# Optimization experiments

Hardware: AMD Instinct MI355X
Metric: run time of the kernel (lower is better)

The kernel has to match this reference:

```python
import jax, jax.numpy as jnp
import numpy as np

N_NODES = 200000
N_EDGES = 4000000
NUM_BASIS = 10
MAX_RADIUS = 1.0
NUM_NEIGHBORS = 10
HIDDEN = 16
# e3nn FCTP(0e+1o+2e, 0e+1o+2e -> 0e): 3 paths (l x l -> 0e), path coeff = 1/sqrt(n_paths*(2l+1))
PATH_C = np.array([1.0 / np.sqrt(3.0 * (2 * l + 1)) for l in (0, 1, 2)], dtype=np.float32)


def _spherical_harmonics_l2(v):
    """e3nn spherical harmonics lmax=2, normalize=True, 'component' normalization. v: [E,3] -> [E,9]."""
    r = jnp.linalg.norm(v, axis=-1, keepdims=True)
    u = v / jnp.maximum(r, 1e-12)
    x, y, z = u[:, 0], u[:, 1], u[:, 2]
    s3, s5 = np.sqrt(3.0).astype(np.float32), np.sqrt(5.0).astype(np.float32)
    sh0 = jnp.ones_like(x)[:, None]                      # [E,1]
    sh1 = s3 * u                                         # [E,3]
    x2, y2, z2 = x * x, y * y, z * z
    sh2 = s5 * jnp.stack([s3 * x * z,
                          s3 * x * y,
                          y2 - 0.5 * (x2 + z2),
                          s3 * y * z,
                          0.5 * s3 * (z2 - x2)], axis=-1)  # [E,5]
    return jnp.concatenate([sh0, sh1, sh2], axis=-1)


def _radial_embedding(r):
    """e3nn soft_one_hot_linspace(basis='smooth_finite', cutoff=True) * sqrt(num_basis). r: [E] -> [E,NUM_BASIS]."""
    values = jnp.linspace(0.0, MAX_RADIUS, NUM_BASIS + 2)[1:-1]
    step = MAX_RADIUS / (NUM_BASIS + 1)
    diff = (r[:, None] - values) / step

    def soft_unit_step(t):
        return jnp.where(t > 0, jnp.exp(-1.0 / jnp.where(t > 0, t, 1.0)), 0.0)

    y = np.float32(1.14136 * np.exp(2.0)) * soft_unit_step(diff + 1.0) * soft_unit_step(1.0 - diff)
    return y * np.float32(np.sqrt(NUM_BASIS))


def setup_inputs() -> dict:
    key = jax.random.key(0)
    k1, k2, k3, k4, k5, k6 = jax.random.split(key, 6)
    node_feats = jax.random.normal(k1, (N_NODES, 9), dtype=jnp.float32)
    edge_vec = 0.25 * jax.random.normal(k2, (N_EDGES, 3), dtype=jnp.float32)  # keep norms mostly < max_radius
    edge_src = jax.random.randint(k3, (N_EDGES,), 0, N_NODES)
    edge_dst = jax.random.randint(k4, (N_EDGES,), 0, N_NODES)
    W1 = jax.random.normal(k5, (NUM_BASIS, HIDDEN), dtype=jnp.float32)
    W2 = jax.random.normal(k6, (HIDDEN, 3), dtype=jnp.float32)
    return {"node_feats": node_feats, "edge_vec": edge_vec, "W1": W1, "W2": W2,
            "edge_src": edge_src, "edge_dst": edge_dst}


def reference(node_feats, edge_vec, W1, W2, edge_src, edge_dst):
    r = jnp.linalg.norm(edge_vec, axis=-1)                      # [E]
    sh = _spherical_harmonics_l2(edge_vec)                      # [E,9]
    emb = _radial_embedding(r)                                  # [E,NUM_BASIS]
    # e3nn FullyConnectedNet([num_basis, 16, 3], relu): variance-preserving layers
    h = np.float32(np.sqrt(2.0)) * jax.nn.relu(emb @ W1 / np.float32(np.sqrt(NUM_BASIS)))
    w = h @ W2 / np.float32(np.sqrt(HIDDEN))                    # [E,3] per-edge TP weights
    f = node_feats[edge_src]                                    # gather [E,9]
    # FCTP paths: l x l -> 0e reduces to per-l dot products
    dots = jnp.stack([f[:, 0] * sh[:, 0],
                      jnp.sum(f[:, 1:4] * sh[:, 1:4], axis=-1),
                      jnp.sum(f[:, 4:9] * sh[:, 4:9], axis=-1)], axis=-1)  # [E,3]
    edge_out = jnp.sum(w * jnp.asarray(PATH_C) * dots, axis=-1)            # [E]
    node_out = jax.ops.segment_sum(edge_out, edge_dst, num_segments=N_NODES)
    node_out = node_out / np.float32(np.sqrt(NUM_NEIGHBORS))
    return node_out.sum()
```

## Files before the change

### kernel.cpp

```cpp
#include <hip/hip_runtime.h>
#include <hip/hip_fp16.h>

#define NTHREADS 256
#define NBLOCKS 2048
#define FB_NBLOCKS 2048
#define NB 1024
#define NBP 1040

#define KTOT 11.9269705f
#define CL0  0.04564355f
#define CL1  0.02635231f
#define CL2  0.02041241f
#define S3   1.7320508f
#define S5   2.2360680f

__device__ __forceinline__ float fast_rcp(float x) { return __builtin_amdgcn_rcpf(x); }

__global__ __launch_bounds__(256) void pack_feats_14(
    const float* __restrict__ nf, uint4* __restrict__ tab, int n_nodes)
{
    const int n = blockIdx.x * 256 + threadIdx.x;
    if (n >= n_nodes) return;
    const float* f = nf + 9 * (size_t)n;
    const float scale[9] = { 1.0f, S3, S3, S3, S5 * S3, S5 * S3, S5, S5 * S3,
                             0.5f * S5 * S3 };
    unsigned short hs[9];
#pragma unroll
    for (int i = 0; i < 9; ++i) {
        const __half h = __float2half_rn(f[i] * scale[i]);
        hs[i] = *reinterpret_cast<const unsigned short*>(&h);
    }
    unsigned long long c[9];
#pragma unroll
    for (int i = 1; i < 9; ++i)
        c[i] = (unsigned long long)(((unsigned)hs[i] + 2u) >> 2) & 0x3FFFull;
    const unsigned long long lo =
        c[1] | (c[2] << 14) | (c[3] << 28) | (c[4] << 42) | (c[5] << 56);
    const unsigned long long hi =
        (c[5] >> 8) | (c[6] << 6) | (c[7] << 20) | (c[8] << 34) |
        ((unsigned long long)hs[0] << 48);
    tab[n] = make_uint4((unsigned)lo, (unsigned)(lo >> 32),
                        (unsigned)hi, (unsigned)(hi >> 32));
}

__global__ __launch_bounds__(256) void build_wtable_kernel(
    const float* __restrict__ W1, const float* __restrict__ W2,
    float* __restrict__ wtabf)
{
    const int idx = blockIdx.x * 256 + threadIdx.x;
    if (idx > NB) return;
    const float r = (float)idx * (1.0f / (float)NB);

    const float t    = 11.0f * r;
    const int   k0   = (int)t;
    const float frac = t - (float)k0;
    float ea = 0.0f, eb = 0.0f;
    if (k0 >= 1 && k0 <= 10) {
        const float da = fmaf(-frac, frac, 1.0f);
        if (da > 0.0226f) ea = KTOT * __expf(-2.0f * fast_rcp(da));
    }
    if (k0 <= 9) {
        const float db = frac * (2.0f - frac);
        if (db > 0.0226f) eb = KTOT * __expf(-2.0f * fast_rcp(db));
    }
    const int ra = min(max(k0 - 1, 0), 9);
    const int rb = min(k0, 9);

    float w0 = 0.0f, w1 = 0.0f, w2 = 0.0f;
#pragma unroll
    for (int j = 0; j < 16; ++j) {
        const float h = fmaxf(fmaf(ea, W1[ra * 16 + j], eb * W1[rb * 16 + j]), 0.0f);
        w0 = fmaf(h, W2[j * 3 + 0], w0);
        w1 = fmaf(h, W2[j * 3 + 1], w1);
        w2 = fmaf(h, W2[j * 3 + 2], w2);
    }
    wtabf[idx]           = w0 * CL0;
    wtabf[NBP + idx]     = w1 * CL1;
    wtabf[2 * NBP + idx] = w2 * CL2;
}

__global__ __launch_bounds__(256) void build_wrec_kernel(
    const float* __restrict__ wtabf, uint4* __restrict__ wrec)
{
    const int i = blockIdx.x * 256 + threadIdx.x;
    if (i >= NB) return;
    const float w0a = wtabf[i],           w0b = wtabf[i + 1];
    const float w1a = wtabf[NBP + i],     w1b = wtabf[NBP + i + 1];
    const float w2a = wtabf[2 * NBP + i], w2b = wtabf[2 * NBP + i + 1];
    auto hbits = [](float v) -> unsigned {
        const __half h = __float2half_rn(v);
        return (unsigned)*reinterpret_cast<const unsigned short*>(&h);
    };
    const unsigned b0 = hbits(w0a), b1 = hbits(w1a), b2 = hbits(w2a);
    const unsigned d0 = hbits(w0b - w0a), d1 = hbits(w1b - w1a), d2 = hbits(w2b - w2a);
    wrec[i] = make_uint4(b0 | (b1 << 16), b2 | (d0 << 16), d1 | (d2 << 16), 0u);
}

__device__ __forceinline__ float cvt14(unsigned c) {
    __half_raw hr; hr.x = (unsigned short)(c << 2);
    return __half2float(*reinterpret_cast<const __half*>(&hr));
}
__device__ __forceinline__ float cvt16(unsigned c) {
    __half_raw hr; hr.x = (unsigned short)(c & 0xFFFFu);
    return __half2float(*reinterpret_cast<const __half*>(&hr));
}
__device__ __forceinline__ unsigned alignb(unsigned hi, unsigned lo, int s) {
    return (lo >> s) | (hi << (32 - s));
}

__device__ __forceinline__ float edge_term(
    float vx, float vy, float vz, uint4 g, const uint4* __restrict__ swq)
{
    const float r2 = fmaf(vx, vx, fmaf(vy, vy, vz * vz));
    const float rs = rsqrtf(fmaxf(r2, 1e-24f));
    const float r  = r2 * rs;
    const float x = vx * rs, y = vy * rs, z = vz * rs;

    const float tb = fminf(r, 1.0f) * (float)NB;
    const int   i  = min((int)tb, NB - 1);
    const float fb = tb - (float)i;
    const uint4 q = swq[i];
    const float wv0 = fmaf(fb, cvt16(q.y >> 16), cvt16(q.x));
    const float wv1 = fmaf(fb, cvt16(q.z),       cvt16(q.x >> 16));
    const float wv2 = fmaf(fb, cvt16(q.z >> 16), cvt16(q.y));

    const float fv1 = cvt14(g.x & 0x3FFFu);
    const float fv2 = cvt14((g.x >> 14) & 0x3FFFu);
    const float fv3 = cvt14(alignb(g.y, g.x, 28) & 0x3FFFu);
    const float fv4 = cvt14((g.y >> 10) & 0x3FFFu);
    const float fv5 = cvt14(alignb(g.z, g.y, 24) & 0x3FFFu);
    const float fv6 = cvt14((g.z >> 6) & 0x3FFFu);
    const float fv7 = cvt14(alignb(g.w, g.z, 20) & 0x3FFFu);
    const float fv8 = cvt14((g.w >> 2) & 0x3FFFu);
    const float f0  = cvt16(g.w >> 16);

    const float dots0 = f0;
    const float dots1 = fmaf(fv1, x, fmaf(fv2, y, fv3 * z));
    const float xx = x * x, yy = y * y, zz = z * z;
    const float dots2 = fmaf(fv4, x * z, fmaf(fv5, x * y,
                        fmaf(fv6, fmaf(-0.5f, xx + zz, yy),
                        fmaf(fv7, y * z, fv8 * (zz - xx)))));

    return fmaf(wv0, dots0, fmaf(wv1, dots1, wv2 * dots2));
}

__global__ __launch_bounds__(NTHREADS) void edge_sum_p14q(
    const float4* __restrict__ ev4,
    const int4*   __restrict__ src4,
    const uint4*  __restrict__ tab,
    const uint4*  __restrict__ wrec,
    float*        __restrict__ block_sums,
    int n_edges)
{
    __shared__ uint4 swq[NB];
    const int tid = threadIdx.x;
    for (int i = tid; i < NB; i += NTHREADS) swq[i] = wrec[i];
    __syncthreads();

    float acc = 0.0f;
    const int n_groups = (n_edges + 3) >> 2;
    const int stride = gridDim.x * blockDim.x;
    for (int g = blockIdx.x * blockDim.x + tid; g < n_groups; g += stride) {
        const int e0 = g << 2;
        if (e0 + 3 < n_edges) {
            const float4 a = ev4[3 * (size_t)g + 0];
            const float4 b = ev4[3 * (size_t)g + 1];
            const float4 c = ev4[3 * (size_t)g + 2];
            const int4   s = src4[g];
            const uint4 g0 = tab[s.x];
            const uint4 g1 = tab[s.y];
            const uint4 g2 = tab[s.z];
            const uint4 g3 = tab[s.w];
            acc += edge_term(a.x, a.y, a.z, g0, swq);
            acc += edge_term(a.w, b.x, b.y, g1, swq);
            acc += edge_term(b.z, b.w, c.x, g2, swq);
            acc += edge_term(c.y, c.z, c.w, g3, swq);
        } else {
            const float* evf  = reinterpret_cast<const float*>(ev4);
            const int*   srci = reinterpret_cast<const int*>(src4);
            for (int e = e0; e < n_edges; ++e) {
                acc += edge_term(evf[3 * (size_t)e], evf[3 * (size_t)e + 1],
                                 evf[3 * (size_t)e + 2], tab[srci[e]], swq);
            }
        }
    }

#pragma unroll
    for (int off = 1; off < 64; off <<= 1)
        acc += __shfl_xor(acc, off, 64);
    __shared__ float wsum[NTHREADS / 64];
    const int lane = tid & 63, wid = tid >> 6;
    if (lane == 0) wsum[wid] = acc;
    __syncthreads();
    if (tid == 0) {
        float ssum = 0.0f;
#pragma unroll
        for (int w = 0; w < NTHREADS / 64; ++w) ssum += wsum[w];
        block_sums[blockIdx.x] = ssum;
    }
}

__global__ __launch_bounds__(NTHREADS) void edge_sum_fallback(
    const float* __restrict__ node_feats,
    const float* __restrict__ edge_vec,
    const float* __restrict__ W1,
    const float* __restrict__ W2,
    const int*   __restrict__ edge_src,
    float*       __restrict__ block_sums,
    int n_edges)
{
    __shared__ float4 sW1[10][5];
    float* sW1f = reinterpret_cast<float*>(sW1);
    const int tid = threadIdx.x;
    if (tid < 160) {
        sW1f[(tid >> 4) * 20 + (tid & 15)] = W1[tid];
    } else if (tid < 200) {
        const int i = tid - 160;
        sW1f[(i >> 2) * 20 + 16 + (i & 3)] = 0.0f;
    }
    __syncthreads();

    float w2r[16][3];
#pragma unroll
    for (int j = 0; j < 16; ++j) {
        w2r[j][0] = W2[j * 3 + 0] * CL0;
        w2r[j][1] = W2[j * 3 + 1] * CL1;
        w2r[j][2] = W2[j * 3 + 2] * CL2;
    }

    float acc = 0.0f;
    const int stride = gridDim.x * blockDim.x;
    for (int e = blockIdx.x * blockDim.x + tid; e < n_edges; e += stride) {
        const float vx = edge_vec[3 * (size_t)e + 0];
        const float vy = edge_vec[3 * (size_t)e + 1];
        const float vz = edge_vec[3 * (size_t)e + 2];
        const int   src = edge_src[e];
        const float* f = node_feats + 9 * (size_t)src;
        const float r2 = fmaf(vx, vx, fmaf(vy, vy, vz * vz));
        const float rs = rsqrtf(fmaxf(r2, 1e-24f));
        const float r  = r2 * rs;
        const float x = vx * rs, y = vy * rs, z = vz * rs;
        const float t    = 11.0f * r;
        const int   k0   = (int)t;
        const float frac = t - (float)k0;
        float ea = 0.0f, eb = 0.0f;
        if (k0 >= 1 && k0 <= 10) {
            const float da = fmaf(-frac, frac, 1.0f);
            if (da > 0.0226f) ea = KTOT * __expf(-2.0f * fast_rcp(da));
        }
        if (k0 <= 9) {
            const float db = frac * (2.0f - frac);
            if (db > 0.0226f) eb = KTOT * __expf(-2.0f * fast_rcp(db));
        }
        const int ra = min(max(k0 - 1, 0), 9);
        const int rb = min(k0, 9);
        const float4* rowA = &sW1[ra][0];
        const float4* rowB = &sW1[rb][0];
        float wv0 = 0.0f, wv1 = 0.0f, wv2 = 0.0f;
#pragma unroll
        for (int q = 0; q < 4; ++q) {
            const float4 A = rowA[q];
            const float4 B = rowB[q];
            float h;
            h = fmaxf(fmaf(ea, A.x, eb * B.x), 0.0f);
            wv0 = fmaf(h, w2r[4 * q + 0][0], wv0); wv1 = fmaf(h, w2r[4 * q + 0][1], wv1); wv2 = fmaf(h, w2r[4 * q + 0][2], wv2);
            h = fmaxf(fmaf(ea, A.y, eb * B.y), 0.0f);
            wv0 = fmaf(h, w2r[4 * q + 1][0], wv0); wv1 = fmaf(h, w2r[4 * q + 1][1], wv1); wv2 = fmaf(h, w2r[4 * q + 1][2], wv2);
            h = fmaxf(fmaf(ea, A.z, eb * B.z), 0.0f);
            wv0 = fmaf(h, w2r[4 * q + 2][0], wv0); wv1 = fmaf(h, w2r[4 * q + 2][1], wv1); wv2 = fmaf(h, w2r[4 * q + 2][2], wv2);
            h = fmaxf(fmaf(ea, A.w, eb * B.w), 0.0f);
            wv0 = fmaf(h, w2r[4 * q + 3][0], wv0); wv1 = fmaf(h, w2r[4 * q + 3][1], wv1); wv2 = fmaf(h, w2r[4 * q + 3][2], wv2);
        }
        const float f0 = f[0], f1 = f[1], f2 = f[2], f3 = f[3], f4 = f[4];
        const float f5 = f[5], f6 = f[6], f7 = f[7], f8 = f[8];
        const float dots0 = f0;
        const float dots1 = S3 * fmaf(f1, x, fmaf(f2, y, f3 * z));
        const float xx = x * x, yy = y * y, zz = z * z;
        const float sh20 = S5 * S3 * x * z;
        const float sh21 = S5 * S3 * x * y;
        const float sh22 = S5 * (yy - 0.5f * (xx + zz));
        const float sh23 = S5 * S3 * y * z;
        const float sh24 = S5 * 0.5f * S3 * (zz - xx);
        const float dots2 = fmaf(f4, sh20, fmaf(f5, sh21, fmaf(f6, sh22, fmaf(f7, sh23, f8 * sh24))));
        acc = fmaf(wv0, dots0, acc);
        acc = fmaf(wv1, dots1, acc);
        acc = fmaf(wv2, dots2, acc);
    }
#pragma unroll
    for (int off = 1; off < 64; off <<= 1)
        acc += __shfl_xor(acc, off, 64);
    __shared__ float wsum[NTHREADS / 64];
    const int lane = tid & 63, wid = tid >> 6;
    if (lane == 0) wsum[wid] = acc;
    __syncthreads();
    if (tid == 0) {
        float ssum = 0.0f;
#pragma unroll
        for (int w = 0; w < NTHREADS / 64; ++w) ssum += wsum[w];
        block_sums[blockIdx.x] = ssum;
    }
}

__global__ __launch_bounds__(256) void final_reduce_kernel(
    const float* __restrict__ block_sums, float* __restrict__ out, int n)
{
    const int tid = threadIdx.x;
    float acc = 0.0f;
    for (int i = tid; i < n; i += 256) acc += block_sums[i];
#pragma unroll
    for (int off = 1; off < 64; off <<= 1)
        acc += __shfl_xor(acc, off, 64);
    __shared__ float wsum[4];
    if ((tid & 63) == 0) wsum[tid >> 6] = acc;
    __syncthreads();
    if (tid == 0) out[0] = wsum[0] + wsum[1] + wsum[2] + wsum[3];
}

extern "C" void kernel_launch(void* const* d_in, const int* in_sizes, int n_in,
                              void* d_out, int out_size, void* d_ws, size_t ws_size,
                              hipStream_t stream) {
    const float* node_feats = (const float*)d_in[0];
    const float* edge_vec   = (const float*)d_in[1];
    const float* W1         = (const float*)d_in[2];
    const float* W2         = (const float*)d_in[3];
    const int*   edge_src   = (const int*)d_in[4];
    const int n_edges = in_sizes[4];
    const int n_nodes = in_sizes[0] / 9;

    float* block_sums = (float*)d_ws;
    const size_t wtabf_off = 32768;
    const size_t wrec_off  = wtabf_off + ((3 * NBP * 4 + 255) & ~255);
    const size_t tab_off   = wrec_off + NB * 16;
    const size_t need      = tab_off + (size_t)n_nodes * 16;

    if (ws_size >= need) {
        float* wtabf = (float*)((char*)d_ws + wtabf_off);
        uint4* wrec  = (uint4*)((char*)d_ws + wrec_off);
        uint4* tab   = (uint4*)((char*)d_ws + tab_off);
        pack_feats_14<<<(n_nodes + 255) / 256, 256, 0, stream>>>(
            node_feats, tab, n_nodes);
        build_wtable_kernel<<<(NB + 256) / 256, 256, 0, stream>>>(W1, W2, wtabf);
        build_wrec_kernel<<<NB / 256, 256, 0, stream>>>(wtabf, wrec);
        edge_sum_p14q<<<NBLOCKS, NTHREADS, 0, stream>>>(
            (const float4*)edge_vec, (const int4*)edge_src, tab, wrec,
            block_sums, n_edges);
        final_reduce_kernel<<<1, 256, 0, stream>>>(block_sums, (float*)d_out, NBLOCKS);
    } else {
        edge_sum_fallback<<<FB_NBLOCKS, NTHREADS, 0, stream>>>(
            node_feats, edge_vec, W1, W2, edge_src, block_sums, n_edges);
        final_reduce_kernel<<<1, 256, 0, stream>>>(block_sums, (float*)d_out, FB_NBLOCKS);
    }
}
```

Before: 46.23 us.

## Fuse prep kernels into one launch and software-pipeline two edge groups

The three setup kernels (feature packing, weight table, and the fp16 base/delta LUT) become a single prep kernel. The LUT blocks recompute the MLP at both endpoints instead of reading an intermediate float table, which removes two launches and one buffer. The edge kernel now issues loads and gathers for its first two grid-stride groups before doing any math, to raise memory-level parallelism on the random node-table gathers. This costs more registers and duplicates the tail-handling code.

```diff
diff --git a/kernel.cpp b/kernel.cpp
--- a/kernel.cpp
+++ b/kernel.cpp
@@ -5,7 +5,6 @@
 #define NBLOCKS 2048
 #define FB_NBLOCKS 2048
 #define NB 1024
-#define NBP 1040
 
 #define KTOT 11.9269705f
 #define CL0  0.04564355f
@@ -16,41 +15,10 @@
 
 __device__ __forceinline__ float fast_rcp(float x) { return __builtin_amdgcn_rcpf(x); }
 
-__global__ __launch_bounds__(256) void pack_feats_14(
-    const float* __restrict__ nf, uint4* __restrict__ tab, int n_nodes)
-{
-    const int n = blockIdx.x * 256 + threadIdx.x;
-    if (n >= n_nodes) return;
-    const float* f = nf + 9 * (size_t)n;
-    const float scale[9] = { 1.0f, S3, S3, S3, S5 * S3, S5 * S3, S5, S5 * S3,
-                             0.5f * S5 * S3 };
-    unsigned short hs[9];
-#pragma unroll
-    for (int i = 0; i < 9; ++i) {
-        const __half h = __float2half_rn(f[i] * scale[i]);
-        hs[i] = *reinterpret_cast<const unsigned short*>(&h);
-    }
-    unsigned long long c[9];
-#pragma unroll
-    for (int i = 1; i < 9; ++i)
-        c[i] = (unsigned long long)(((unsigned)hs[i] + 2u) >> 2) & 0x3FFFull;
-    const unsigned long long lo =
-        c[1] | (c[2] << 14) | (c[3] << 28) | (c[4] << 42) | (c[5] << 56);
-    const unsigned long long hi =
-        (c[5] >> 8) | (c[6] << 6) | (c[7] << 20) | (c[8] << 34) |
-        ((unsigned long long)hs[0] << 48);
-    tab[n] = make_uint4((unsigned)lo, (unsigned)(lo >> 32),
-                        (unsigned)hi, (unsigned)(hi >> 32));
-}
-
-__global__ __launch_bounds__(256) void build_wtable_kernel(
-    const float* __restrict__ W1, const float* __restrict__ W2,
-    float* __restrict__ wtabf)
-{
-    const int idx = blockIdx.x * 256 + threadIdx.x;
-    if (idx > NB) return;
-    const float r = (float)idx * (1.0f / (float)NB);
-
+__device__ __forceinline__ void eval_w(
+    float r, const float* __restrict__ W1, const float* __restrict__ W2,
+    float& w0, float& w1, float& w2)
+{
     const float t    = 11.0f * r;
     const int   k0   = (int)t;
     const float frac = t - (float)k0;
@@ -65,8 +33,7 @@
     }
     const int ra = min(max(k0 - 1, 0), 9);
     const int rb = min(k0, 9);
-
-    float w0 = 0.0f, w1 = 0.0f, w2 = 0.0f;
+    w0 = 0.0f; w1 = 0.0f; w2 = 0.0f;
 #pragma unroll
     for (int j = 0; j < 16; ++j) {
         const float h = fmaxf(fmaf(ea, W1[ra * 16 + j], eb * W1[rb * 16 + j]), 0.0f);
@@ -74,26 +41,53 @@
         w1 = fmaf(h, W2[j * 3 + 1], w1);
         w2 = fmaf(h, W2[j * 3 + 2], w2);
     }
-    wtabf[idx]           = w0 * CL0;
-    wtabf[NBP + idx]     = w1 * CL1;
-    wtabf[2 * NBP + idx] = w2 * CL2;
-}
-
-__global__ __launch_bounds__(256) void build_wrec_kernel(
-    const float* __restrict__ wtabf, uint4* __restrict__ wrec)
-{
-    const int i = blockIdx.x * 256 + threadIdx.x;
-    if (i >= NB) return;
-    const float w0a = wtabf[i],           w0b = wtabf[i + 1];
-    const float w1a = wtabf[NBP + i],     w1b = wtabf[NBP + i + 1];
-    const float w2a = wtabf[2 * NBP + i], w2b = wtabf[2 * NBP + i + 1];
-    auto hbits = [](float v) -> unsigned {
-        const __half h = __float2half_rn(v);
-        return (unsigned)*reinterpret_cast<const unsigned short*>(&h);
-    };
-    const unsigned b0 = hbits(w0a), b1 = hbits(w1a), b2 = hbits(w2a);
-    const unsigned d0 = hbits(w0b - w0a), d1 = hbits(w1b - w1a), d2 = hbits(w2b - w2a);
-    wrec[i] = make_uint4(b0 | (b1 << 16), b2 | (d0 << 16), d1 | (d2 << 16), 0u);
+    w0 *= CL0; w1 *= CL1; w2 *= CL2;
+}
+
+__global__ __launch_bounds__(256) void prep_kernel(
+    const float* __restrict__ nf,
+    const float* __restrict__ W1, const float* __restrict__ W2,
+    uint4* __restrict__ tab, uint4* __restrict__ wrec,
+    int n_nodes, int pack_blocks)
+{
+    const int tid = threadIdx.x;
+    if ((int)blockIdx.x < pack_blocks) {
+        const int n = blockIdx.x * 256 + tid;
+        if (n >= n_nodes) return;
+        const float* f = nf + 9 * (size_t)n;
+        const float scale[9] = { 1.0f, S3, S3, S3, S5 * S3, S5 * S3, S5, S5 * S3,
+                                 0.5f * S5 * S3 };
+        unsigned short hs[9];
+#pragma unroll
+        for (int i = 0; i < 9; ++i) {
+            const __half h = __float2half_rn(f[i] * scale[i]);
+            hs[i] = *reinterpret_cast<const unsigned short*>(&h);
+        }
+        unsigned long long c[9];
+#pragma unroll
+        for (int i = 1; i < 9; ++i)
+            c[i] = (unsigned long long)(((unsigned)hs[i] + 2u) >> 2) & 0x3FFFull;
+        const unsigned long long lo =
+            c[1] | (c[2] << 14) | (c[3] << 28) | (c[4] << 42) | (c[5] << 56);
+        const unsigned long long hi =
+            (c[5] >> 8) | (c[6] << 6) | (c[7] << 20) | (c[8] << 34) |
+            ((unsigned long long)hs[0] << 48);
+        tab[n] = make_uint4((unsigned)lo, (unsigned)(lo >> 32),
+                            (unsigned)hi, (unsigned)(hi >> 32));
+    } else {
+        const int i = ((int)blockIdx.x - pack_blocks) * 256 + tid;
+        if (i >= NB) return;
+        float w0a, w1a, w2a, w0b, w1b, w2b;
+        eval_w((float)i       * (1.0f / (float)NB), W1, W2, w0a, w1a, w2a);
+        eval_w((float)(i + 1) * (1.0f / (float)NB), W1, W2, w0b, w1b, w2b);
+        auto hbits = [](float v) -> unsigned {
+            const __half h = __float2half_rn(v);
+            return (unsigned)*reinterpret_cast<const unsigned short*>(&h);
+        };
+        const unsigned b0 = hbits(w0a), b1 = hbits(w1a), b2 = hbits(w2a);
+        const unsigned d0 = hbits(w0b - w0a), d1 = hbits(w1b - w1a), d2 = hbits(w2b - w2a);
+        wrec[i] = make_uint4(b0 | (b1 << 16), b2 | (d0 << 16), d1 | (d2 << 16), 0u);
+    }
 }
 
 __device__ __forceinline__ float cvt14(unsigned c) {
@@ -144,7 +138,7 @@
     return fmaf(wv0, dots0, fmaf(wv1, dots1, wv2 * dots2));
 }
 
-__global__ __launch_bounds__(NTHREADS) void edge_sum_p14q(
+__global__ __launch_bounds__(NTHREADS) void edge_sum_u2(
     const float4* __restrict__ ev4,
     const int4*   __restrict__ src4,
     const uint4*  __restrict__ tab,
@@ -160,29 +154,77 @@
     float acc = 0.0f;
     const int n_groups = (n_edges + 3) >> 2;
     const int stride = gridDim.x * blockDim.x;
-    for (int g = blockIdx.x * blockDim.x + tid; g < n_groups; g += stride) {
+    const int g1 = blockIdx.x * blockDim.x + tid;
+    const int g2 = g1 + stride;
+    const bool v1 = (g1 < n_groups) && ((g1 << 2) + 4 <= n_edges);
+    const bool v2 = (g2 < n_groups) && ((g2 << 2) + 4 <= n_edges);
+
+    float4 a1, b1, c1, a2, b2, c2;
+    int4 s1, s2;
+    if (v1) {
+        a1 = ev4[3 * (size_t)g1 + 0];
+        b1 = ev4[3 * (size_t)g1 + 1];
+        c1 = ev4[3 * (size_t)g1 + 2];
+        s1 = src4[g1];
+    }
+    if (v2) {
+        a2 = ev4[3 * (size_t)g2 + 0];
+        b2 = ev4[3 * (size_t)g2 + 1];
+        c2 = ev4[3 * (size_t)g2 + 2];
+        s2 = src4[g2];
+    }
+    uint4 t0, t1, t2, t3, t4, t5, t6, t7;
+    if (v1) { t0 = tab[s1.x]; t1 = tab[s1.y]; t2 = tab[s1.z]; t3 = tab[s1.w]; }
+    if (v2) { t4 = tab[s2.x]; t5 = tab[s2.y]; t6 = tab[s2.z]; t7 = tab[s2.w]; }
+    if (v1) {
+        acc += edge_term(a1.x, a1.y, a1.z, t0, swq);
+        acc += edge_term(a1.w, b1.x, b1.y, t1, swq);
+        acc += edge_term(b1.z, b1.w, c1.x, t2, swq);
+        acc += edge_term(c1.y, c1.z, c1.w, t3, swq);
+    }
+    if (v2) {
+        acc += edge_term(a2.x, a2.y, a2.z, t4, swq);
+        acc += edge_term(a2.w, b2.x, b2.y, t5, swq);
+        acc += edge_term(b2.z, b2.w, c2.x, t6, swq);
+        acc += edge_term(c2.y, c2.z, c2.w, t7, swq);
+    }
+
+    for (int g = g1 + 2 * stride; g < n_groups; g += stride) {
         const int e0 = g << 2;
-        if (e0 + 3 < n_edges) {
+        if (e0 + 4 <= n_edges) {
             const float4 a = ev4[3 * (size_t)g + 0];
             const float4 b = ev4[3 * (size_t)g + 1];
             const float4 c = ev4[3 * (size_t)g + 2];
             const int4   s = src4[g];
-            const uint4 g0 = tab[s.x];
-            const uint4 g1 = tab[s.y];
-            const uint4 g2 = tab[s.z];
-            const uint4 g3 = tab[s.w];
-            acc += edge_term(a.x, a.y, a.z, g0, swq);
-            acc += edge_term(a.w, b.x, b.y, g1, swq);
-            acc += edge_term(b.z, b.w, c.x, g2, swq);
-            acc += edge_term(c.y, c.z, c.w, g3, swq);
+            const uint4 q0 = tab[s.x];
+            const uint4 q1 = tab[s.y];
+            const uint4 q2 = tab[s.z];
+            const uint4 q3 = tab[s.w];
+            acc += edge_term(a.x, a.y, a.z, q0, swq);
+            acc += edge_term(a.w, b.x, b.y, q1, swq);
+            acc += edge_term(b.z, b.w, c.x, q2, swq);
+            acc += edge_term(c.y, c.z, c.w, q3, swq);
         } else {
             const float* evf  = reinterpret_cast<const float*>(ev4);
             const int*   srci = reinterpret_cast<const int*>(src4);
-            for (int e = e0; e < n_edges; ++e) {
+            for (int e = e0; e < n_edges; ++e)
                 acc += edge_term(evf[3 * (size_t)e], evf[3 * (size_t)e + 1],
                                  evf[3 * (size_t)e + 2], tab[srci[e]], swq);
-            }
-        }
+        }
+    }
+    if (g1 < n_groups && !v1) {
+        const float* evf  = reinterpret_cast<const float*>(ev4);
+        const int*   srci = reinterpret_cast<const int*>(src4);
+        for (int e = (g1 << 2); e < n_edges; ++e)
+            acc += edge_term(evf[3 * (size_t)e], evf[3 * (size_t)e + 1],
+                             evf[3 * (size_t)e + 2], tab[srci[e]], swq);
+    }
+    if (g2 < n_groups && !v2) {
+        const float* evf  = reinterpret_cast<const float*>(ev4);
+        const int*   srci = reinterpret_cast<const int*>(src4);
+        for (int e = (g2 << 2); e < n_edges; ++e)
+            acc += edge_term(evf[3 * (size_t)e], evf[3 * (size_t)e + 1],
+                             evf[3 * (size_t)e + 2], tab[srci[e]], swq);
     }
 
 #pragma unroll
@@ -328,20 +370,18 @@
     const int n_nodes = in_sizes[0] / 9;
 
     float* block_sums = (float*)d_ws;
-    const size_t wtabf_off = 32768;
-    const size_t wrec_off  = wtabf_off + ((3 * NBP * 4 + 255) & ~255);
-    const size_t tab_off   = wrec_off + NB * 16;
-    const size_t need      = tab_off + (size_t)n_nodes * 16;
+    const size_t wrec_off = 32768;
+    const size_t tab_off  = wrec_off + NB * 16;
+    const size_t need     = tab_off + (size_t)n_nodes * 16;
 
     if (ws_size >= need) {
-        float* wtabf = (float*)((char*)d_ws + wtabf_off);
-        uint4* wrec  = (uint4*)((char*)d_ws + wrec_off);
-        uint4* tab   = (uint4*)((char*)d_ws + tab_off);
-        pack_feats_14<<<(n_nodes + 255) / 256, 256, 0, stream>>>(
-            node_feats, tab, n_nodes);
-        build_wtable_kernel<<<(NB + 256) / 256, 256, 0, stream>>>(W1, W2, wtabf);
-        build_wrec_kernel<<<NB / 256, 256, 0, stream>>>(wtabf, wrec);
-        edge_sum_p14q<<<NBLOCKS, NTHREADS, 0, stream>>>(
+        uint4* wrec = (uint4*)((char*)d_ws + wrec_off);
+        uint4* tab  = (uint4*)((char*)d_ws + tab_off);
+        const int pack_blocks = (n_nodes + 255) / 256;
+        const int lut_blocks  = NB / 256;
+        prep_kernel<<<pack_blocks + lut_blocks, 256, 0, stream>>>(
+            node_feats, W1, W2, tab, wrec, n_nodes, pack_blocks);
+        edge_sum_u2<<<NBLOCKS, NTHREADS, 0, stream>>>(
             (const float4*)edge_vec, (const int4*)edge_src, tab, wrec,
             block_sums, n_edges);
         final_reduce_kernel<<<1, 256, 0, stream>>>(block_sums, (float*)d_out, NBLOCKS);
```

Measured after the change: 44.80 us. 3.1% less time.

## Merge prep kernels into one launch, use nontemporal streaming loads and raw rsq

Applied to the files above, without the earlier changes.

Folds the node-feature packing, radial weight table build and delta-record build into a single prep kernel. The LUT blocks now evaluate the MLP directly at both interval ends instead of going through an intermediate float table. This removes two kernel launches and their serialisation gaps. The edge kernel reads edge vectors and source indices with nontemporal loads so the streaming data does not evict the gathered node table from cache, and it uses the raw v_rsq instruction instead of rsqrtf. The cost is duplicated MLP evaluation per LUT entry and a slight change in rsqrt accuracy.

```diff
diff --git a/kernel.cpp b/kernel.cpp
--- a/kernel.cpp
+++ b/kernel.cpp
@@ -5,7 +5,6 @@
 #define NBLOCKS 2048
 #define FB_NBLOCKS 2048
 #define NB 1024
-#define NBP 1040
 
 #define KTOT 11.9269705f
 #define CL0  0.04564355f
@@ -15,42 +14,27 @@
 #define S5   2.2360680f
 
 __device__ __forceinline__ float fast_rcp(float x) { return __builtin_amdgcn_rcpf(x); }
-
-__global__ __launch_bounds__(256) void pack_feats_14(
-    const float* __restrict__ nf, uint4* __restrict__ tab, int n_nodes)
-{
-    const int n = blockIdx.x * 256 + threadIdx.x;
-    if (n >= n_nodes) return;
-    const float* f = nf + 9 * (size_t)n;
-    const float scale[9] = { 1.0f, S3, S3, S3, S5 * S3, S5 * S3, S5, S5 * S3,
-                             0.5f * S5 * S3 };
-    unsigned short hs[9];
-#pragma unroll
-    for (int i = 0; i < 9; ++i) {
-        const __half h = __float2half_rn(f[i] * scale[i]);
-        hs[i] = *reinterpret_cast<const unsigned short*>(&h);
-    }
-    unsigned long long c[9];
-#pragma unroll
-    for (int i = 1; i < 9; ++i)
-        c[i] = (unsigned long long)(((unsigned)hs[i] + 2u) >> 2) & 0x3FFFull;
-    const unsigned long long lo =
-        c[1] | (c[2] << 14) | (c[3] << 28) | (c[4] << 42) | (c[5] << 56);
-    const unsigned long long hi =
-        (c[5] >> 8) | (c[6] << 6) | (c[7] << 20) | (c[8] << 34) |
-        ((unsigned long long)hs[0] << 48);
-    tab[n] = make_uint4((unsigned)lo, (unsigned)(lo >> 32),
-                        (unsigned)hi, (unsigned)(hi >> 32));
-}
-
-__global__ __launch_bounds__(256) void build_wtable_kernel(
-    const float* __restrict__ W1, const float* __restrict__ W2,
-    float* __restrict__ wtabf)
-{
-    const int idx = blockIdx.x * 256 + threadIdx.x;
-    if (idx > NB) return;
-    const float r = (float)idx * (1.0f / (float)NB);
-
+__device__ __forceinline__ float fast_rsq(float x) {
+    float r;
+    asm("v_rsq_f32 %0, %1" : "=v"(r) : "v"(x));
+    return r;
+}
+
+typedef float    vf4 __attribute__((ext_vector_type(4)));
+typedef int      vi4 __attribute__((ext_vector_type(4)));
+__device__ __forceinline__ float4 ntload4(const float4* p) {
+    vf4 v = __builtin_nontemporal_load((const vf4*)p);
+    return make_float4(v.x, v.y, v.z, v.w);
+}
+__device__ __forceinline__ int4 ntloadi4(const int4* p) {
+    vi4 v = __builtin_nontemporal_load((const vi4*)p);
+    return make_int4(v.x, v.y, v.z, v.w);
+}
+
+__device__ __forceinline__ void eval_w(
+    float r, const float* __restrict__ W1, const float* __restrict__ W2,
+    float& w0, float& w1, float& w2)
+{
     const float t    = 11.0f * r;
     const int   k0   = (int)t;
     const float frac = t - (float)k0;
@@ -65,8 +49,7 @@
     }
     const int ra = min(max(k0 - 1, 0), 9);
     const int rb = min(k0, 9);
-
-    float w0 = 0.0f, w1 = 0.0f, w2 = 0.0f;
+    w0 = 0.0f; w1 = 0.0f; w2 = 0.0f;
 #pragma unroll
     for (int j = 0; j < 16; ++j) {
         const float h = fmaxf(fmaf(ea, W1[ra * 16 + j], eb * W1[rb * 16 + j]), 0.0f);
@@ -74,26 +57,53 @@
         w1 = fmaf(h, W2[j * 3 + 1], w1);
         w2 = fmaf(h, W2[j * 3 + 2], w2);
     }
-    wtabf[idx]           = w0 * CL0;
-    wtabf[NBP + idx]     = w1 * CL1;
-    wtabf[2 * NBP + idx] = w2 * CL2;
-}
-
-__global__ __launch_bounds__(256) void build_wrec_kernel(
-    const float* __restrict__ wtabf, uint4* __restrict__ wrec)
-{
-    const int i = blockIdx.x * 256 + threadIdx.x;
-    if (i >= NB) return;
-    const float w0a = wtabf[i],           w0b = wtabf[i + 1];
-    const float w1a = wtabf[NBP + i],     w1b = wtabf[NBP + i + 1];
-    const float w2a = wtabf[2 * NBP + i], w2b = wtabf[2 * NBP + i + 1];
-    auto hbits = [](float v) -> unsigned {
-        const __half h = __float2half_rn(v);
-        return (unsigned)*reinterpret_cast<const unsigned short*>(&h);
-    };
-    const unsigned b0 = hbits(w0a), b1 = hbits(w1a), b2 = hbits(w2a);
-    const unsigned d0 = hbits(w0b - w0a), d1 = hbits(w1b - w1a), d2 = hbits(w2b - w2a);
-    wrec[i] = make_uint4(b0 | (b1 << 16), b2 | (d0 << 16), d1 | (d2 << 16), 0u);
+    w0 *= CL0; w1 *= CL1; w2 *= CL2;
+}
+
+__global__ __launch_bounds__(256) void prep_kernel(
+    const float* __restrict__ nf,
+    const float* __restrict__ W1, const float* __restrict__ W2,
+    uint4* __restrict__ tab, uint4* __restrict__ wrec,
+    int n_nodes, int pack_blocks)
+{
+    const int tid = threadIdx.x;
+    if ((int)blockIdx.x < pack_blocks) {
+        const int n = blockIdx.x * 256 + tid;
+        if (n >= n_nodes) return;
+        const float* f = nf + 9 * (size_t)n;
+        const float scale[9] = { 1.0f, S3, S3, S3, S5 * S3, S5 * S3, S5, S5 * S3,
+                                 0.5f * S5 * S3 };
+        unsigned short hs[9];
+#pragma unroll
+        for (int i = 0; i < 9; ++i) {
+            const __half h = __float2half_rn(f[i] * scale[i]);
+            hs[i] = *reinterpret_cast<const unsigned short*>(&h);
+        }
+        unsigned long long c[9];
+#pragma unroll
+        for (int i = 1; i < 9; ++i)
+            c[i] = (unsigned long long)(((unsigned)hs[i] + 2u) >> 2) & 0x3FFFull;
+        const unsigned long long lo =
+            c[1] | (c[2] << 14) | (c[3] << 28) | (c[4] << 42) | (c[5] << 56);
+        const unsigned long long hi =
+            (c[5] >> 8) | (c[6] << 6) | (c[7] << 20) | (c[8] << 34) |
+            ((unsigned long long)hs[0] << 48);
+        tab[n] = make_uint4((unsigned)lo, (unsigned)(lo >> 32),
+                            (unsigned)hi, (unsigned)(hi >> 32));
+    } else {
+        const int i = ((int)blockIdx.x - pack_blocks) * 256 + tid;
+        if (i >= NB) return;
+        float w0a, w1a, w2a, w0b, w1b, w2b;
+        eval_w((float)i       * (1.0f / (float)NB), W1, W2, w0a, w1a, w2a);
+        eval_w((float)(i + 1) * (1.0f / (float)NB), W1, W2, w0b, w1b, w2b);
+        auto hbits = [](float v) -> unsigned {
+            const __half h = __float2half_rn(v);
+            return (unsigned)*reinterpret_cast<const unsigned short*>(&h);
+        };
+        const unsigned b0 = hbits(w0a), b1 = hbits(w1a), b2 = hbits(w2a);
+        const unsigned d0 = hbits(w0b - w0a), d1 = hbits(w1b - w1a), d2 = hbits(w2b - w2a);
+        wrec[i] = make_uint4(b0 | (b1 << 16), b2 | (d0 << 16), d1 | (d2 << 16), 0u);
+    }
 }
 
 __device__ __forceinline__ float cvt14(unsigned c) {
@@ -112,7 +122,7 @@
     float vx, float vy, float vz, uint4 g, const uint4* __restrict__ swq)
 {
     const float r2 = fmaf(vx, vx, fmaf(vy, vy, vz * vz));
-    const float rs = rsqrtf(fmaxf(r2, 1e-24f));
+    const float rs = fast_rsq(fmaxf(r2, 1e-24f));
     const float r  = r2 * rs;
     const float x = vx * rs, y = vy * rs, z = vz * rs;
 
@@ -144,7 +154,7 @@
     return fmaf(wv0, dots0, fmaf(wv1, dots1, wv2 * dots2));
 }
 
-__global__ __launch_bounds__(NTHREADS) void edge_sum_p14q(
+__global__ __launch_bounds__(NTHREADS) void edge_sum_nt(
     const float4* __restrict__ ev4,
     const int4*   __restrict__ src4,
     const uint4*  __restrict__ tab,
@@ -163,10 +173,10 @@
     for (int g = blockIdx.x * blockDim.x + tid; g < n_groups; g += stride) {
         const int e0 = g << 2;
         if (e0 + 3 < n_edges) {
-            const float4 a = ev4[3 * (size_t)g + 0];
-            const float4 b = ev4[3 * (size_t)g + 1];
-            const float4 c = ev4[3 * (size_t)g + 2];
-            const int4   s = src4[g];
+            const float4 a = ntload4(ev4 + 3 * (size_t)g + 0);
+            const float4 b = ntload4(ev4 + 3 * (size_t)g + 1);
+            const float4 c = ntload4(ev4 + 3 * (size_t)g + 2);
+            const int4   s = ntloadi4(src4 + g);
             const uint4 g0 = tab[s.x];
             const uint4 g1 = tab[s.y];
             const uint4 g2 = tab[s.z];
@@ -328,20 +338,18 @@
     const int n_nodes = in_sizes[0] / 9;
 
     float* block_sums = (float*)d_ws;
-    const size_t wtabf_off = 32768;
-    const size_t wrec_off  = wtabf_off + ((3 * NBP * 4 + 255) & ~255);
-    const size_t tab_off   = wrec_off + NB * 16;
-    const size_t need      = tab_off + (size_t)n_nodes * 16;
+    const size_t wrec_off = 32768;
+    const size_t tab_off  = wrec_off + NB * 16;
+    const size_t need     = tab_off + (size_t)n_nodes * 16;
 
     if (ws_size >= need) {
-        float* wtabf = (float*)((char*)d_ws + wtabf_off);
-        uint4* wrec  = (uint4*)((char*)d_ws + wrec_off);
-        uint4* tab   = (uint4*)((char*)d_ws + tab_off);
-        pack_feats_14<<<(n_nodes + 255) / 256, 256, 0, stream>>>(
-            node_feats, tab, n_nodes);
-        build_wtable_kernel<<<(NB + 256) / 256, 256, 0, stream>>>(W1, W2, wtabf);
-        build_wrec_kernel<<<NB / 256, 256, 0, stream>>>(wtabf, wrec);
-        edge_sum_p14q<<<NBLOCKS, NTHREADS, 0, stream>>>(
+        uint4* wrec = (uint4*)((char*)d_ws + wrec_off);
+        uint4* tab  = (uint4*)((char*)d_ws + tab_off);
+        const int pack_blocks = (n_nodes + 255) / 256;
+        const int lut_blocks  = NB / 256;
+        prep_kernel<<<pack_blocks + lut_blocks, 256, 0, stream>>>(
+            node_feats, W1, W2, tab, wrec, n_nodes, pack_blocks);
+        edge_sum_nt<<<NBLOCKS, NTHREADS, 0, stream>>>(
             (const float4*)edge_vec, (const int4*)edge_src, tab, wrec,
             block_sums, n_edges);
         final_reduce_kernel<<<1, 256, 0, stream>>>(block_sums, (float*)d_out, NBLOCKS);
```

Result: slower. 50.60 us (+9.5%).
